# Kernel optimization log

Hardware: AMD Instinct MI355X
Metric: run time of the kernel (lower is better)

## Reference

```python
import jax, jax.numpy as jnp
import numpy as np

STAGE = 100  # number of weight bins


def _bin_reconstruct(w, affine):
    # Faithful vectorization of the 100-iter binning loop: element in bin i
    # (half-open interval) gets scaled by affine[i]; the max element falls
    # outside every bin (w < wmin + stage*range/stage fails) and is zeroed.
    flat = w.reshape(-1)
    wmin, wmax = flat.min(), flat.max()
    idx = jnp.floor((flat - wmin) / (wmax - wmin) * STAGE).astype(jnp.int32)
    mask = (idx < STAGE).astype(flat.dtype)  # mask is detached in torch (non-diff anyway)
    scale = affine[jnp.clip(idx, 0, STAGE - 1)]
    return flat * scale * mask


def _kl_vs_laplace(new_flat, lap):
    # F.kl_div(log_softmax(w), softmax(lap), reduction='none').mean()
    logq = jax.nn.log_softmax(new_flat)
    p = jax.nn.softmax(lap)
    return (p * (jnp.log(p) - logq)).mean()


def _adder2d(x, w, stride, padding, groups=1):
    # AdderNet conv: out = -sum_k |patch_k - w_k| (no bias)
    O, Cg, kh, kw = w.shape
    patches = jax.lax.conv_general_dilated_patches(
        x, (kh, kw), (stride, stride), [(padding, padding), (padding, padding)])
    B, _, Hp, Wp = patches.shape  # channel dim ordered (C, kh, kw), C-major
    if groups == 1:
        p = patches.reshape(B, 1, Cg * kh * kw, Hp, Wp)
        wf = w.reshape(1, O, Cg * kh * kw, 1, 1)
    else:  # depthwise: groups == C_in, Cg == 1, O == C_in
        p = patches.reshape(B, O, kh * kw, Hp, Wp)
        wf = w.reshape(1, O, kh * kw, 1, 1)
    return -jnp.abs(p - wf).sum(axis=2)  # [B, O, Hp, Wp]


def _bn_train(x, g, b, eps=1e-5):
    # BatchNorm2d in training mode (batch statistics, biased variance)
    m = x.mean(axis=(0, 2, 3), keepdims=True)
    v = ((x - m) ** 2).mean(axis=(0, 2, 3), keepdims=True)
    return (x - m) * jax.lax.rsqrt(v + eps) * g.reshape(1, -1, 1, 1) + b.reshape(1, -1, 1, 1)


def _forward(x, sw_ds, sw_c1, sw_c2, sw_c3, a_ds, a_c1, a_c2, a_c3, peg_w,
             g1, b1, g2, b2, g3, b3, gds, bds, lap_ds, lap_c1, lap_c2, lap_c3):
    kl = jnp.float32(0.0)
    f_ds = _bin_reconstruct(sw_ds, a_ds)
    kl = kl + _kl_vs_laplace(f_ds, lap_ds)
    f_c1 = _bin_reconstruct(sw_c1, a_c1)
    kl = kl + _kl_vs_laplace(f_c1, lap_c1)
    residual = jax.nn.relu(_bn_train(_adder2d(x, f_ds.reshape(sw_ds.shape), 1, 0), gds, bds))
    h = _adder2d(x, f_c1.reshape(sw_c1.shape), 1, 0)
    h = _adder2d(h, peg_w, 1, 1, groups=peg_w.shape[0])  # PEG depthwise 3x3
    h = jax.nn.relu(_bn_train(h, g1, b1))
    f_c2 = _bin_reconstruct(sw_c2, a_c2)
    kl = kl + _kl_vs_laplace(f_c2, lap_c2)
    h = _adder2d(h, f_c2.reshape(sw_c2.shape), 1, 1)
    h = jax.nn.relu(_bn_train(h, g2, b2))
    f_c3 = _bin_reconstruct(sw_c3, a_c3)
    kl = kl + _kl_vs_laplace(f_c3, lap_c3)
    h = _adder2d(h, f_c3.reshape(sw_c3.shape), 1, 0)
    h = _bn_train(h, g3, b3)  # bn3 gamma zero-initialized
    return jax.nn.relu(h + residual), kl


def setup_inputs() -> dict:
    key = jax.random.key(0)
    ks = jax.random.split(key, 16)
    inp = {
        'x': jax.random.normal(ks[0], (4, 128, 28, 28), jnp.float32),
        'sw_downsample': jax.random.normal(ks[1], (256, 128, 1, 1), jnp.float32) * 0.05,
        'sw_conv1': jax.random.normal(ks[2], (64, 128, 1, 1), jnp.float32) * 0.05,
        'sw_conv2': jax.random.normal(ks[3], (64, 64, 3, 3), jnp.float32) * 0.05,
        'sw_conv3': jax.random.normal(ks[4], (256, 64, 1, 1), jnp.float32) * 0.05,
        'downsample_affine': jax.random.normal(ks[5], (100,), jnp.float32),
        'conv1_affine': jax.random.normal(ks[6], (100,), jnp.float32),
        'conv2_affine': jax.random.normal(ks[7], (100,), jnp.float32),
        'conv3_affine': jax.random.normal(ks[8], (100,), jnp.float32),
        'peg_w': jax.random.normal(ks[9], (64, 1, 3, 3), jnp.float32) * 0.05,
        'bn1_g': jnp.ones((64,), jnp.float32), 'bn1_b': jnp.zeros((64,), jnp.float32),
        'bn2_g': jnp.ones((64,), jnp.float32), 'bn2_b': jnp.zeros((64,), jnp.float32),
        'bn3_g': jnp.zeros((256,), jnp.float32), 'bn3_b': jnp.zeros((256,), jnp.float32),
        'bnds_g': jnp.ones((256,), jnp.float32), 'bnds_b': jnp.zeros((256,), jnp.float32),
        # Laplace(0, 2) samples, drawn once in setup so the reference is deterministic
        'lap_ds': jax.random.laplace(ks[10], (32768,), jnp.float32) * 2.0,
        'lap_c1': jax.random.laplace(ks[11], (8192,), jnp.float32) * 2.0,
        'lap_c2': jax.random.laplace(ks[12], (36864,), jnp.float32) * 2.0,
        'lap_c3': jax.random.laplace(ks[13], (16384,), jnp.float32) * 2.0,
    }
    return inp


def reference(x, sw_downsample, sw_conv1, sw_conv2, sw_conv3,
              downsample_affine, conv1_affine, conv2_affine, conv3_affine, peg_w,
              bn1_g, bn1_b, bn2_g, bn2_b, bn3_g, bn3_b, bnds_g, bnds_b,
              lap_ds, lap_c1, lap_c2, lap_c3):
    return _forward(x, sw_downsample, sw_conv1, sw_conv2, sw_conv3,
                    downsample_affine, conv1_affine, conv2_affine, conv3_affine, peg_w,
                    bn1_g, bn1_b, bn2_g, bn2_b, bn3_g, bn3_b, bnds_g, bnds_b,
                    lap_ds, lap_c1, lap_c2, lap_c3)
```

## Files before the change

kernel.cpp:

```cpp
#include <hip/hip_runtime.h>
#include <math.h>


#define HW 784
#define NB 4
#define STAGE 100

__device__ __forceinline__ float wredSum(float v){
  for (int o = 32; o > 0; o >>= 1) v += __shfl_down(v, o, 64);
  return v;
}
__device__ __forceinline__ float wredMax(float v){
  for (int o = 32; o > 0; o >>= 1) v = fmaxf(v, __shfl_down(v, o, 64));
  return v;
}
__device__ __forceinline__ float wredMin(float v){
  for (int o = 32; o > 0; o >>= 1) v = fminf(v, __shfl_down(v, o, 64));
  return v;
}
__device__ __forceinline__ double wredSumD(double v){
  for (int o = 32; o > 0; o >>= 1) v += __shfl_down(v, o, 64);
  return v;
}

__device__ float blockMin4(float v){
  __shared__ float shn[4];
  __syncthreads();
  v = wredMin(v);
  if ((threadIdx.x & 63) == 0) shn[threadIdx.x >> 6] = v;
  __syncthreads();
  return fminf(fminf(shn[0], shn[1]), fminf(shn[2], shn[3]));
}
__device__ float blockMax4(float v){
  __shared__ float shx[4];
  __syncthreads();
  v = wredMax(v);
  if ((threadIdx.x & 63) == 0) shx[threadIdx.x >> 6] = v;
  __syncthreads();
  return fmaxf(fmaxf(shx[0], shx[1]), fmaxf(shx[2], shx[3]));
}

__device__ void stats4(float v0, float v1, float v2, float v3,
                       double* sumP, double* sqP, int oc0){
  __shared__ double sred[4][8];
  __syncthreads();
  const int w = threadIdx.x >> 6;
  float vv[4] = {v0, v1, v2, v3};
  #pragma unroll
  for (int i = 0; i < 4; i++){
    double d = (double)vv[i];
    double s = wredSumD(d);
    double q = wredSumD(d * d);
    if ((threadIdx.x & 63) == 0){ sred[w][i] = s; sred[w][4 + i] = q; }
  }
  __syncthreads();
  if (threadIdx.x < 8){
    double tot = sred[0][threadIdx.x] + sred[1][threadIdx.x]
               + sred[2][threadIdx.x] + sred[3][threadIdx.x];
    int i = threadIdx.x & 3;
    if (threadIdx.x < 4) atomicAdd(&sumP[oc0 + i], tot);
    else                 atomicAdd(&sqP[oc0 + i],  tot);
  }
}
__device__ void stats2(float v0, float v1, double* sumP, double* sqP, int oc0){
  __shared__ double sred2[4][4];
  __syncthreads();
  const int w = threadIdx.x >> 6;
  float vv[2] = {v0, v1};
  #pragma unroll
  for (int i = 0; i < 2; i++){
    double d = (double)vv[i];
    double s = wredSumD(d);
    double q = wredSumD(d * d);
    if ((threadIdx.x & 63) == 0){ sred2[w][i] = s; sred2[w][2 + i] = q; }
  }
  __syncthreads();
  if (threadIdx.x < 4){
    double tot = sred2[0][threadIdx.x] + sred2[1][threadIdx.x]
               + sred2[2][threadIdx.x] + sred2[3][threadIdx.x];
    int i = threadIdx.x & 1;
    if (threadIdx.x < 2) atomicAdd(&sumP[oc0 + i], tot);
    else                 atomicAdd(&sqP[oc0 + i],  tot);
  }
}

__device__ void klAccum(float se, float sel, float sef, float sq, double* dst){
  __shared__ double kls[4][4];
  __syncthreads();
  const int w = threadIdx.x >> 6;
  double a0 = wredSumD((double)se);
  double a1 = wredSumD((double)sel);
  double a2 = wredSumD((double)sef);
  double a3 = wredSumD((double)sq);
  if ((threadIdx.x & 63) == 0){
    kls[w][0] = a0; kls[w][1] = a1; kls[w][2] = a2; kls[w][3] = a3;
  }
  __syncthreads();
  if (threadIdx.x < 4){
    double tot = kls[0][threadIdx.x] + kls[1][threadIdx.x]
               + kls[2][threadIdx.x] + kls[3][threadIdx.x];
    atomicAdd(&dst[threadIdx.x], tot);
  }
}

__device__ __forceinline__ float reconv(float vv, float mn, float rng,
                                        const float* saff){
  float q = (vv - mn) / rng * 100.0f;
  int idx = (int)floorf(q);
  float nv = 0.0f;
  if (idx < STAGE){
    int ci = idx < 0 ? 0 : (idx > STAGE - 1 ? STAGE - 1 : idx);
    nv = vv * saff[ci];
  }
  return nv;
}

__device__ __forceinline__ void mmReduce(const float* mmbuf, int tens,
                                         float& mn, float& mx){
  mn = 3.402823466e38f; mx = -3.402823466e38f;
  #pragma unroll
  for (int k = 0; k < 16; k++){
    mn = fminf(mn, mmbuf[tens * 32 + k]);
    mx = fmaxf(mx, mmbuf[tens * 32 + 16 + k]);
  }
}

__global__ __launch_bounds__(256) void minmax_kernel(
    const float* w0, int n0, const float* w1, int n1,
    const float* w2, int n2, const float* w3, int n3,
    float* mmbuf, double* dstat)
{
  if (threadIdx.x < 21) dstat[blockIdx.x * 21 + threadIdx.x] = 0.0;
  const int tens = blockIdx.x >> 4, slot = blockIdx.x & 15;
  const float* w; int n;
  if      (tens == 0){ w = w0; n = n0; }
  else if (tens == 1){ w = w1; n = n1; }
  else if (tens == 2){ w = w2; n = n2; }
  else               { w = w3; n = n3; }
  float mn = 3.402823466e38f, mx = -3.402823466e38f;
  for (int i = slot * 256 + threadIdx.x; i < n; i += 4096){
    float v = w[i];
    mn = fminf(mn, v); mx = fmaxf(mx, v);
  }
  mn = blockMin4(mn); mx = blockMax4(mx);
  if (threadIdx.x == 0){
    mmbuf[tens * 32 + slot]      = mn;
    mmbuf[tens * 32 + 16 + slot] = mx;
  }
}

__global__ __launch_bounds__(256) void front_kernel(
    const float* __restrict__ x,
    const float* __restrict__ w_ds, const float* __restrict__ aff_ds,
    const float* __restrict__ lap_ds,
    const float* __restrict__ w_c1, const float* __restrict__ aff_c1,
    const float* __restrict__ lap_c1,
    const float* __restrict__ w_c2, const float* __restrict__ aff_c2,
    const float* __restrict__ lap_c2, float* __restrict__ f_c2,
    const float* __restrict__ w_c3, const float* __restrict__ aff_c3,
    const float* __restrict__ lap_c3,
    const float* __restrict__ peg_w, const float* __restrict__ mmbuf,
    float* __restrict__ A, float* __restrict__ T2, double* __restrict__ dS)
{
  const int t = threadIdx.x;
  if (blockIdx.x < 512){
    const int a = blockIdx.x;
    const int chunk = a & 3, og = (a >> 2) & 31, b = a >> 7;
    const int oc0 = og * 8;
    __shared__ float saff[STAGE];
    __shared__ float sw[1024];
    if (t < STAGE) saff[t] = aff_ds[t];
    float mn, mx; mmReduce(mmbuf, 0, mn, mx);
    const float rng = mx - mn;
    __syncthreads();
    for (int k = t; k < 1024; k += 256)
      sw[k] = reconv(w_ds[oc0 * 128 + k], mn, rng, saff);
    __syncthreads();

    const int px = chunk * 196 + t;
    float v0=0,v1=0,v2=0,v3=0,v4=0,v5=0,v6=0,v7=0;
    if (t < 196){
      const float* xp = x + (size_t)b * 128 * HW + px;
      float c0=0,c1=0,c2=0,c3=0,c4=0,c5=0,c6=0,c7=0;
      #pragma unroll 4
      for (int c = 0; c < 128; c++){
        float xv = xp[(size_t)c * HW];
        c0 += fabsf(xv - sw[c]);
        c1 += fabsf(xv - sw[128 + c]);
        c2 += fabsf(xv - sw[256 + c]);
        c3 += fabsf(xv - sw[384 + c]);
        c4 += fabsf(xv - sw[512 + c]);
        c5 += fabsf(xv - sw[640 + c]);
        c6 += fabsf(xv - sw[768 + c]);
        c7 += fabsf(xv - sw[896 + c]);
      }
      v0=-c0; v1=-c1; v2=-c2; v3=-c3; v4=-c4; v5=-c5; v6=-c6; v7=-c7;
      float* op = A + ((size_t)(b * 256 + oc0)) * HW + px;
      op[0]=v0; op[HW]=v1; op[2*HW]=v2; op[3*HW]=v3;
      op[4*HW]=v4; op[5*HW]=v5; op[6*HW]=v6; op[7*HW]=v7;
    }
    stats4(v0, v1, v2, v3, dS + 0, dS + 256, oc0);
    stats4(v4, v5, v6, v7, dS + 0, dS + 256, oc0 + 4);

    if (b == 0 && chunk == 0){
      float se = 0, sel = 0, sef = 0, sq = 0;
      for (int k = t; k < 1024; k += 256){
        float l = lap_ds[oc0 * 128 + k];
        float e = expf(l);
        se += e; sel += e * l; sef += e * sw[k];
        sq += expf(sw[k]);
      }
      klAccum(se, sel, sef, sq, dS + 1280 + 0);
    }
  } else if (blockIdx.x < 768){
    const int a = blockIdx.x - 512;
    const int rc = a & 3, og = (a >> 2) & 15, b = a >> 6;
    const int oc0 = og * 4;
    __shared__ float saffc[STAGE];
    __shared__ float swc[512];
    __shared__ float swp[36];
    __shared__ float sT1[4][256];
    if (t < STAGE) saffc[t] = aff_c1[t];
    if (t >= 128 && t < 164) swp[t - 128] = peg_w[oc0 * 9 + (t - 128)];
    float mn, mx; mmReduce(mmbuf, 1, mn, mx);
    const float rng = mx - mn;
    __syncthreads();
    for (int k = t; k < 512; k += 256)
      swc[k] = reconv(w_c1[oc0 * 128 + k], mn, rng, saffc);
    __syncthreads();

    if (t < 252){
      const int rr = t / 28;
      const int col = t - rr * 28;
      const int wr = rc * 7 - 1 + rr;
      float tv0 = 0, tv1 = 0, tv2 = 0, tv3 = 0;
      if (wr >= 0 && wr < 28){
        const float* xp = x + (size_t)b * 128 * HW + wr * 28 + col;
        float c0 = 0, c1 = 0, c2 = 0, c3 = 0;
        #pragma unroll 4
        for (int c = 0; c < 128; c++){
          float xv = xp[(size_t)c * HW];
          c0 += fabsf(xv - swc[c]);
          c1 += fabsf(xv - swc[128 + c]);
          c2 += fabsf(xv - swc[256 + c]);
          c3 += fabsf(xv - swc[384 + c]);
        }
        tv0 = -c0; tv1 = -c1; tv2 = -c2; tv3 = -c3;
      }
      sT1[0][t] = tv0; sT1[1][t] = tv1; sT1[2][t] = tv2; sT1[3][t] = tv3;
    }
    __syncthreads();
    float v0 = 0, v1 = 0, v2 = 0, v3 = 0;
    if (t < 196){
      const int r = t / 28, col = t - r * 28;
      float c0 = 0, c1 = 0, c2 = 0, c3 = 0;
      #pragma unroll
      for (int ky = 0; ky < 3; ky++){
        #pragma unroll
        for (int kx = 0; kx < 3; kx++){
          int cc = col + kx - 1;
          bool ok = (cc >= 0) && (cc < 28);
          int idx = ok ? ((r + ky) * 28 + cc) : 0;
          float p0 = ok ? sT1[0][idx] : 0.0f;
          float p1 = ok ? sT1[1][idx] : 0.0f;
          float p2 = ok ? sT1[2][idx] : 0.0f;
          float p3 = ok ? sT1[3][idx] : 0.0f;
          int wk = ky * 3 + kx;
          c0 += fabsf(p0 - swp[wk]);
          c1 += fabsf(p1 - swp[9 + wk]);
          c2 += fabsf(p2 - swp[18 + wk]);
          c3 += fabsf(p3 - swp[27 + wk]);
        }
      }
      v0 = -c0; v1 = -c1; v2 = -c2; v3 = -c3;
      const int opx = (rc * 7 + r) * 28 + col;
      float* op = T2 + ((size_t)(b * 64 + oc0)) * HW + opx;
      op[0] = v0; op[HW] = v1; op[2 * HW] = v2; op[3 * HW] = v3;
    }
    stats4(v0, v1, v2, v3, dS + 512, dS + 576, oc0);

    if (b == 0 && rc == 0){
      float se = 0, sel = 0, sef = 0, sq = 0;
      for (int k = t; k < 512; k += 256){
        float l = lap_c1[oc0 * 128 + k];
        float e = expf(l);
        se += e; sel += e * l; sef += e * swc[k];
        sq += expf(swc[k]);
      }
      klAccum(se, sel, sef, sq, dS + 1280 + 4);
    }
  } else if (blockIdx.x < 832){
    const int j = blockIdx.x - 768;
    __shared__ float saff2[STAGE];
    if (t < STAGE) saff2[t] = aff_c2[t];
    float mn, mx; mmReduce(mmbuf, 2, mn, mx);
    const float rng = mx - mn;
    __syncthreads();
    float se = 0, sel = 0, sef = 0, sq = 0;
    for (int k = t; k < 576; k += 256){
      float nv = reconv(w_c2[j * 576 + k], mn, rng, saff2);
      f_c2[j * 576 + k] = nv;
      float l = lap_c2[j * 576 + k];
      float e = expf(l);
      se += e; sel += e * l; sef += e * nv; sq += expf(nv);
    }
    klAccum(se, sel, sef, sq, dS + 1280 + 8);
  } else {
    const int j = blockIdx.x - 832;
    __shared__ float saff3[STAGE];
    if (t < STAGE) saff3[t] = aff_c3[t];
    float mn, mx; mmReduce(mmbuf, 3, mn, mx);
    const float rng = mx - mn;
    __syncthreads();
    float se = 0, sel = 0, sef = 0, sq = 0;
    for (int k = t; k < 1024; k += 256){
      float nv = reconv(w_c3[j * 1024 + k], mn, rng, saff3);
      float l = lap_c3[j * 1024 + k];
      float e = expf(l);
      se += e; sel += e * l; sef += e * nv; sq += expf(nv);
    }
    klAccum(se, sel, sef, sq, dS + 1280 + 12);
  }
}

__global__ __launch_bounds__(256) void bnapply_pad_kernel(
    const float* __restrict__ T2, float* __restrict__ T2b,
    const float* __restrict__ g1, const float* __restrict__ b1,
    const double* __restrict__ dS)
{
  const int a = blockIdx.x;
  const int c = a & 63, b = a >> 6;
  __shared__ float ssc, ssb;
  if (threadIdx.x == 0){
    double s  = dS[512 + c] * (1.0 / 3136.0);
    double vr = dS[576 + c] * (1.0 / 3136.0) - s * s;
    float scale = g1[c] * rsqrtf((float)vr + 1e-5f);
    ssc = scale; ssb = b1[c] - (float)s * scale;
  }
  __syncthreads();
  const float sc_ = ssc, bi_ = ssb;
  const float* src = T2 + (size_t)a * HW;
  float* dst = T2b + (size_t)a * 960;
  for (int i = threadIdx.x; i < 960; i += 256){
    int row = i >> 5, col = i & 31;
    float v = 0.0f;
    if (row >= 1 && row <= 28 && col >= 1 && col <= 28)
      v = fmaxf(src[(row - 1) * 28 + (col - 1)] * sc_ + bi_, 0.0f);
    dst[i] = v;
  }
}

__global__ __launch_bounds__(256) void mid3x3_kernel(
    const float* __restrict__ T2b, const float* __restrict__ f_c2,
    float* __restrict__ T3, double* __restrict__ dS)
{
  const int t = threadIdx.x;
  const int a = blockIdx.x;
  const int chunk = a & 3, og = (a >> 2) & 31, b = a >> 7;
  const int oc0 = og * 2;
  const float* __restrict__ wA = f_c2 + oc0 * 576;
  const float* __restrict__ wB = wA + 576;

  float v0 = 0, v1 = 0;
  const int px = chunk * 196 + t;
  if (t < 196){
    const int y = px / 28, xc = px - y * 28;
    const float* base = T2b + (size_t)b * 64 * 960 + y * 32 + xc;
    float c0 = 0, c1 = 0;
    #pragma unroll 2
    for (int c = 0; c < 64; c++){
      const float* p = base + c * 960;
      float t0 = p[0],  t1 = p[1],  t2 = p[2];
      float t3 = p[32], t4 = p[33], t5 = p[34];
      float t6 = p[64], t7 = p[65], t8 = p[66];
      const float* wa = wA + c * 9;
      const float* wb = wB + c * 9;
      c0 += fabsf(t0 - wa[0]) + fabsf(t1 - wa[1]) + fabsf(t2 - wa[2])
          + fabsf(t3 - wa[3]) + fabsf(t4 - wa[4]) + fabsf(t5 - wa[5])
          + fabsf(t6 - wa[6]) + fabsf(t7 - wa[7]) + fabsf(t8 - wa[8]);
      c1 += fabsf(t0 - wb[0]) + fabsf(t1 - wb[1]) + fabsf(t2 - wb[2])
          + fabsf(t3 - wb[3]) + fabsf(t4 - wb[4]) + fabsf(t5 - wb[5])
          + fabsf(t6 - wb[6]) + fabsf(t7 - wb[7]) + fabsf(t8 - wb[8]);
    }
    v0 = -c0; v1 = -c1;
    T3[((size_t)(b * 64 + oc0)) * HW + px]     = v0;
    T3[((size_t)(b * 64 + oc0 + 1)) * HW + px] = v1;
  }
  stats2(v0, v1, dS + 640, dS + 704, oc0);
}

__global__ __launch_bounds__(256) void back_kernel(
    const float* __restrict__ T3, const float* __restrict__ w_c3,
    const float* __restrict__ aff_c3, const float* __restrict__ mmbuf,
    const float* __restrict__ g2, const float* __restrict__ b2,
    float* __restrict__ out, double* __restrict__ dS)
{
  const int t = threadIdx.x;
  const int a = blockIdx.x;
  const int chunk = a & 3, og = (a >> 2) & 63, b = a >> 8;
  const int oc0 = og * 4;
  __shared__ float ssc[64], ssb[64], sw[256], saff[STAGE];
  if (t < 64){
    double s  = dS[640 + t] * (1.0 / 3136.0);
    double vr = dS[704 + t] * (1.0 / 3136.0) - s * s;
    float scale = g2[t] * rsqrtf((float)vr + 1e-5f);
    ssc[t] = scale; ssb[t] = b2[t] - (float)s * scale;
  }
  if (t >= 128 && t < 128 + STAGE) saff[t - 128] = aff_c3[t - 128];
  float mn, mx; mmReduce(mmbuf, 3, mn, mx);
  const float rng = mx - mn;
  __syncthreads();
  sw[t] = reconv(w_c3[oc0 * 64 + t], mn, rng, saff);
  __syncthreads();

  const int px = chunk * 196 + t;
  float v0 = 0, v1 = 0, v2 = 0, v3 = 0;
  if (t < 196){
    const float* bp = T3 + (size_t)b * 64 * HW + px;
    float c0 = 0, c1 = 0, c2 = 0, c3 = 0;
    #pragma unroll 4
    for (int c = 0; c < 64; c++){
      float raw = bp[(size_t)c * HW];
      float vv = fmaxf(raw * ssc[c] + ssb[c], 0.0f);
      c0 += fabsf(vv - sw[c]);
      c1 += fabsf(vv - sw[64 + c]);
      c2 += fabsf(vv - sw[128 + c]);
      c3 += fabsf(vv - sw[192 + c]);
    }
    v0 = -c0; v1 = -c1; v2 = -c2; v3 = -c3;
    float* op = out + ((size_t)(b * 256 + oc0)) * HW + px;
    op[0] = v0; op[HW] = v1; op[2 * HW] = v2; op[3 * HW] = v3;
  }
  stats4(v0, v1, v2, v3, dS + 768, dS + 1024, oc0);
}

__global__ __launch_bounds__(256) void final_kernel(
    float* __restrict__ out, const float* __restrict__ A,
    const float* __restrict__ g3, const float* __restrict__ b3,
    const float* __restrict__ gds, const float* __restrict__ bds,
    const double* __restrict__ dS)
{
  __shared__ float s3c[256], s3b[256], sdc[256], sdb[256];
  const int t = threadIdx.x;
  {
    double s  = dS[768 + t] * (1.0 / 3136.0);
    double vr = dS[1024 + t] * (1.0 / 3136.0) - s * s;
    float scale = g3[t] * rsqrtf((float)vr + 1e-5f);
    s3c[t] = scale; s3b[t] = b3[t] - (float)s * scale;
    s  = dS[t] * (1.0 / 3136.0);
    vr = dS[256 + t] * (1.0 / 3136.0) - s * s;
    scale = gds[t] * rsqrtf((float)vr + 1e-5f);
    sdc[t] = scale; sdb[t] = bds[t] - (float)s * scale;
  }
  __syncthreads();
  #pragma unroll
  for (int k = 0; k < 4; k++){
    int n = blockIdx.x * 1024 + k * 256 + t;
    int c = (n / HW) & 255;
    float h = out[n], aa = A[n];
    float r = fmaxf(aa * sdc[c] + sdb[c], 0.0f);
    out[n] = fmaxf(h * s3c[c] + s3b[c] + r, 0.0f);
  }
  if (blockIdx.x == 0 && t == 0){
    const int ns[4] = {32768, 8192, 36864, 16384};
    float kl = 0.0f;
    #pragma unroll
    for (int q = 0; q < 4; q++){
      double se  = dS[1280 + q * 4];
      double sel = dS[1280 + q * 4 + 1];
      double sef = dS[1280 + q * 4 + 2];
      double sq  = dS[1280 + q * 4 + 3];
      kl += (float)((((sel - sef) / se) - log(se) + log(sq)) / (double)ns[q]);
    }
    out[802816] = kl;
  }
}

extern "C" void kernel_launch(void* const* d_in, const int* in_sizes, int n_in,
                              void* d_out, int out_size, void* d_ws, size_t ws_size,
                              hipStream_t stream)
{
  const float* x      = (const float*)d_in[0];
  const float* sw_ds  = (const float*)d_in[1];
  const float* sw_c1  = (const float*)d_in[2];
  const float* sw_c2  = (const float*)d_in[3];
  const float* sw_c3  = (const float*)d_in[4];
  const float* a_ds   = (const float*)d_in[5];
  const float* a_c1   = (const float*)d_in[6];
  const float* a_c2   = (const float*)d_in[7];
  const float* a_c3   = (const float*)d_in[8];
  const float* peg_w  = (const float*)d_in[9];
  const float* bn1_g  = (const float*)d_in[10];
  const float* bn1_b  = (const float*)d_in[11];
  const float* bn2_g  = (const float*)d_in[12];
  const float* bn2_b  = (const float*)d_in[13];
  const float* bn3_g  = (const float*)d_in[14];
  const float* bn3_b  = (const float*)d_in[15];
  const float* bnds_g = (const float*)d_in[16];
  const float* bnds_b = (const float*)d_in[17];
  const float* lap_ds = (const float*)d_in[18];
  const float* lap_c1 = (const float*)d_in[19];
  const float* lap_c2 = (const float*)d_in[20];
  const float* lap_c3 = (const float*)d_in[21];

  float* ws    = (float*)d_ws;
  float* f_c2  = ws;
  float* mmbuf = ws + 36864;
  double* dstat= (double*)(ws + 37120);
  float* A     = ws + 39808;
  float* T2    = ws + 842624;
  float* T3    = ws + 1043328;
  float* T2b   = ws + 1244032;

  float* out = (float*)d_out;

  minmax_kernel<<<64, 256, 0, stream>>>(
      sw_ds, 32768, sw_c1, 8192, sw_c2, 36864, sw_c3, 16384, mmbuf, dstat);

  front_kernel<<<848, 256, 0, stream>>>(
      x, sw_ds, a_ds, lap_ds, sw_c1, a_c1, lap_c1,
      sw_c2, a_c2, lap_c2, f_c2, sw_c3, a_c3, lap_c3,
      peg_w, mmbuf, A, T2, dstat);

  bnapply_pad_kernel<<<256, 256, 0, stream>>>(T2, T2b, bn1_g, bn1_b, dstat);

  mid3x3_kernel<<<512, 256, 0, stream>>>(T2b, f_c2, T3, dstat);

  back_kernel<<<1024, 256, 0, stream>>>(T3, sw_c3, a_c3, mmbuf,
                                        bn2_g, bn2_b, out, dstat);

  final_kernel<<<784, 256, 0, stream>>>(out, A, bn3_g, bn3_b, bnds_g, bnds_b,
                                        dstat);
}
```

Measured before the change: 171.8 us.

## Precompute reconstructed weights once in transposed layout and drop per-block requantization

Replaces the min/max kernel with one kernel that computes each weight tensor's full min/max per block, reconstructs the binned weights once, stores them transposed (input-channel-major) in workspace, and writes per-block KL partial sums without atomics. The conv kernels now read the transposed weights straight from global memory instead of rebuilding them in shared memory in every block. This removes redundant reconstruction work and several barriers per block. In exchange, every block of the reconstruction kernel rescans its whole tensor for min/max, and the inner loops take uniform global loads in place of LDS reads, which relies on caching.

```diff
diff --git a/kernel.cpp b/kernel.cpp
--- a/kernel.cpp
+++ b/kernel.cpp
@@ -6,10 +6,6 @@
 #define NB 4
 #define STAGE 100
 
-__device__ __forceinline__ float wredSum(float v){
-  for (int o = 32; o > 0; o >>= 1) v += __shfl_down(v, o, 64);
-  return v;
-}
 __device__ __forceinline__ float wredMax(float v){
   for (int o = 32; o > 0; o >>= 1) v = fmaxf(v, __shfl_down(v, o, 64));
   return v;
@@ -84,25 +80,6 @@
   }
 }
 
-__device__ void klAccum(float se, float sel, float sef, float sq, double* dst){
-  __shared__ double kls[4][4];
-  __syncthreads();
-  const int w = threadIdx.x >> 6;
-  double a0 = wredSumD((double)se);
-  double a1 = wredSumD((double)sel);
-  double a2 = wredSumD((double)sef);
-  double a3 = wredSumD((double)sq);
-  if ((threadIdx.x & 63) == 0){
-    kls[w][0] = a0; kls[w][1] = a1; kls[w][2] = a2; kls[w][3] = a3;
-  }
-  __syncthreads();
-  if (threadIdx.x < 4){
-    double tot = kls[0][threadIdx.x] + kls[1][threadIdx.x]
-               + kls[2][threadIdx.x] + kls[3][threadIdx.x];
-    atomicAdd(&dst[threadIdx.x], tot);
-  }
-}
-
 __device__ __forceinline__ float reconv(float vv, float mn, float rng,
                                         const float* saff){
   float q = (vv - mn) / rng * 100.0f;
@@ -115,51 +92,75 @@
   return nv;
 }
 
-__device__ __forceinline__ void mmReduce(const float* mmbuf, int tens,
-                                         float& mn, float& mx){
-  mn = 3.402823466e38f; mx = -3.402823466e38f;
-  #pragma unroll
-  for (int k = 0; k < 16; k++){
-    mn = fminf(mn, mmbuf[tens * 32 + k]);
-    mx = fmaxf(mx, mmbuf[tens * 32 + 16 + k]);
-  }
-}
-
-__global__ __launch_bounds__(256) void minmax_kernel(
-    const float* w0, int n0, const float* w1, int n1,
-    const float* w2, int n2, const float* w3, int n3,
-    float* mmbuf, double* dstat)
-{
-  if (threadIdx.x < 21) dstat[blockIdx.x * 21 + threadIdx.x] = 0.0;
-  const int tens = blockIdx.x >> 4, slot = blockIdx.x & 15;
-  const float* w; int n;
-  if      (tens == 0){ w = w0; n = n0; }
-  else if (tens == 1){ w = w1; n = n1; }
-  else if (tens == 2){ w = w2; n = n2; }
-  else               { w = w3; n = n3; }
+__global__ __launch_bounds__(256) void reconkl_kernel(
+    const float* __restrict__ w_ds, const float* __restrict__ a_ds,
+    const float* __restrict__ lap_ds, float* __restrict__ f_dsT,
+    const float* __restrict__ w_c1, const float* __restrict__ a_c1,
+    const float* __restrict__ lap_c1, float* __restrict__ f_c1T,
+    const float* __restrict__ w_c2, const float* __restrict__ a_c2,
+    const float* __restrict__ lap_c2, float* __restrict__ f_c2,
+    const float* __restrict__ w_c3, const float* __restrict__ a_c3,
+    const float* __restrict__ lap_c3, float* __restrict__ f_c3T,
+    double* __restrict__ dstat)
+{
+  const int blk = blockIdx.x, t = threadIdx.x;
+  if (t < 14 && blk * 14 + t < 1280) dstat[blk * 14 + t] = 0.0;
+
+  int tens, slice;
+  if      (blk < 32){ tens = 0; slice = blk; }
+  else if (blk < 40){ tens = 1; slice = blk - 32; }
+  else if (blk < 76){ tens = 2; slice = blk - 40; }
+  else              { tens = 3; slice = blk - 76; }
+  const float *w, *aff, *lap; int n;
+  if      (tens == 0){ w = w_ds; aff = a_ds; lap = lap_ds; n = 32768; }
+  else if (tens == 1){ w = w_c1; aff = a_c1; lap = lap_c1; n = 8192; }
+  else if (tens == 2){ w = w_c2; aff = a_c2; lap = lap_c2; n = 36864; }
+  else               { w = w_c3; aff = a_c3; lap = lap_c3; n = 16384; }
+
+  __shared__ float saff[STAGE];
+  if (t < STAGE) saff[t] = aff[t];
+
+  const float4* w4 = (const float4*)w;
   float mn = 3.402823466e38f, mx = -3.402823466e38f;
-  for (int i = slot * 256 + threadIdx.x; i < n; i += 4096){
-    float v = w[i];
-    mn = fminf(mn, v); mx = fmaxf(mx, v);
+  for (int i = t; i < (n >> 2); i += 256){
+    float4 v = w4[i];
+    mn = fminf(mn, fminf(fminf(v.x, v.y), fminf(v.z, v.w)));
+    mx = fmaxf(mx, fmaxf(fmaxf(v.x, v.y), fmaxf(v.z, v.w)));
   }
   mn = blockMin4(mn); mx = blockMax4(mx);
-  if (threadIdx.x == 0){
-    mmbuf[tens * 32 + slot]      = mn;
-    mmbuf[tens * 32 + 16 + slot] = mx;
+  const float rng = mx - mn;
+
+  float se = 0, sel = 0, sef = 0, sq = 0;
+  const int k0 = slice * 1024;
+  for (int j = t; j < 1024; j += 256){
+    int k = k0 + j;
+    float nv = reconv(w[k], mn, rng, saff);
+    if      (tens == 0){ int oc = k >> 7, c = k & 127; f_dsT[c * 256 + oc] = nv; }
+    else if (tens == 1){ int oc = k >> 7, c = k & 127; f_c1T[c * 64 + oc] = nv; }
+    else if (tens == 2){ f_c2[k] = nv; }
+    else               { int oc = k >> 6, c = k & 63;  f_c3T[c * 256 + oc] = nv; }
+    float l = lap[k];
+    float e = expf(l);
+    se += e; sel += e * l; sef += e * nv; sq += expf(nv);
+  }
+  __shared__ double kls[4][4];
+  __syncthreads();
+  const int wv = t >> 6;
+  double a0 = wredSumD((double)se);
+  double a1 = wredSumD((double)sel);
+  double a2 = wredSumD((double)sef);
+  double a3 = wredSumD((double)sq);
+  if ((t & 63) == 0){ kls[wv][0]=a0; kls[wv][1]=a1; kls[wv][2]=a2; kls[wv][3]=a3; }
+  __syncthreads();
+  if (t < 4){
+    double tot = kls[0][t] + kls[1][t] + kls[2][t] + kls[3][t];
+    dstat[1280 + blk * 4 + t] = tot;
   }
 }
 
 __global__ __launch_bounds__(256) void front_kernel(
-    const float* __restrict__ x,
-    const float* __restrict__ w_ds, const float* __restrict__ aff_ds,
-    const float* __restrict__ lap_ds,
-    const float* __restrict__ w_c1, const float* __restrict__ aff_c1,
-    const float* __restrict__ lap_c1,
-    const float* __restrict__ w_c2, const float* __restrict__ aff_c2,
-    const float* __restrict__ lap_c2, float* __restrict__ f_c2,
-    const float* __restrict__ w_c3, const float* __restrict__ aff_c3,
-    const float* __restrict__ lap_c3,
-    const float* __restrict__ peg_w, const float* __restrict__ mmbuf,
+    const float* __restrict__ x, const float* __restrict__ f_dsT,
+    const float* __restrict__ f_c1T, const float* __restrict__ peg_w,
     float* __restrict__ A, float* __restrict__ T2, double* __restrict__ dS)
 {
   const int t = threadIdx.x;
@@ -167,32 +168,24 @@
     const int a = blockIdx.x;
     const int chunk = a & 3, og = (a >> 2) & 31, b = a >> 7;
     const int oc0 = og * 8;
-    __shared__ float saff[STAGE];
-    __shared__ float sw[1024];
-    if (t < STAGE) saff[t] = aff_ds[t];
-    float mn, mx; mmReduce(mmbuf, 0, mn, mx);
-    const float rng = mx - mn;
-    __syncthreads();
-    for (int k = t; k < 1024; k += 256)
-      sw[k] = reconv(w_ds[oc0 * 128 + k], mn, rng, saff);
-    __syncthreads();
-
     const int px = chunk * 196 + t;
     float v0=0,v1=0,v2=0,v3=0,v4=0,v5=0,v6=0,v7=0;
     if (t < 196){
       const float* xp = x + (size_t)b * 128 * HW + px;
+      const float* wp = f_dsT + oc0;
       float c0=0,c1=0,c2=0,c3=0,c4=0,c5=0,c6=0,c7=0;
       #pragma unroll 4
       for (int c = 0; c < 128; c++){
         float xv = xp[(size_t)c * HW];
-        c0 += fabsf(xv - sw[c]);
-        c1 += fabsf(xv - sw[128 + c]);
-        c2 += fabsf(xv - sw[256 + c]);
-        c3 += fabsf(xv - sw[384 + c]);
-        c4 += fabsf(xv - sw[512 + c]);
-        c5 += fabsf(xv - sw[640 + c]);
-        c6 += fabsf(xv - sw[768 + c]);
-        c7 += fabsf(xv - sw[896 + c]);
+        const float* wr = wp + c * 256;
+        c0 += fabsf(xv - wr[0]);
+        c1 += fabsf(xv - wr[1]);
+        c2 += fabsf(xv - wr[2]);
+        c3 += fabsf(xv - wr[3]);
+        c4 += fabsf(xv - wr[4]);
+        c5 += fabsf(xv - wr[5]);
+        c6 += fabsf(xv - wr[6]);
+        c7 += fabsf(xv - wr[7]);
       }
       v0=-c0; v1=-c1; v2=-c2; v3=-c3; v4=-c4; v5=-c5; v6=-c6; v7=-c7;
       float* op = A + ((size_t)(b * 256 + oc0)) * HW + px;
@@ -201,34 +194,11 @@
     }
     stats4(v0, v1, v2, v3, dS + 0, dS + 256, oc0);
     stats4(v4, v5, v6, v7, dS + 0, dS + 256, oc0 + 4);
-
-    if (b == 0 && chunk == 0){
-      float se = 0, sel = 0, sef = 0, sq = 0;
-      for (int k = t; k < 1024; k += 256){
-        float l = lap_ds[oc0 * 128 + k];
-        float e = expf(l);
-        se += e; sel += e * l; sef += e * sw[k];
-        sq += expf(sw[k]);
-      }
-      klAccum(se, sel, sef, sq, dS + 1280 + 0);
-    }
-  } else if (blockIdx.x < 768){
+  } else {
     const int a = blockIdx.x - 512;
     const int rc = a & 3, og = (a >> 2) & 15, b = a >> 6;
     const int oc0 = og * 4;
-    __shared__ float saffc[STAGE];
-    __shared__ float swc[512];
-    __shared__ float swp[36];
     __shared__ float sT1[4][256];
-    if (t < STAGE) saffc[t] = aff_c1[t];
-    if (t >= 128 && t < 164) swp[t - 128] = peg_w[oc0 * 9 + (t - 128)];
-    float mn, mx; mmReduce(mmbuf, 1, mn, mx);
-    const float rng = mx - mn;
-    __syncthreads();
-    for (int k = t; k < 512; k += 256)
-      swc[k] = reconv(w_c1[oc0 * 128 + k], mn, rng, saffc);
-    __syncthreads();
-
     if (t < 252){
       const int rr = t / 28;
       const int col = t - rr * 28;
@@ -236,14 +206,16 @@
       float tv0 = 0, tv1 = 0, tv2 = 0, tv3 = 0;
       if (wr >= 0 && wr < 28){
         const float* xp = x + (size_t)b * 128 * HW + wr * 28 + col;
+        const float* wp = f_c1T + oc0;
         float c0 = 0, c1 = 0, c2 = 0, c3 = 0;
         #pragma unroll 4
         for (int c = 0; c < 128; c++){
           float xv = xp[(size_t)c * HW];
-          c0 += fabsf(xv - swc[c]);
-          c1 += fabsf(xv - swc[128 + c]);
-          c2 += fabsf(xv - swc[256 + c]);
-          c3 += fabsf(xv - swc[384 + c]);
+          const float* wrp = wp + c * 64;
+          c0 += fabsf(xv - wrp[0]);
+          c1 += fabsf(xv - wrp[1]);
+          c2 += fabsf(xv - wrp[2]);
+          c3 += fabsf(xv - wrp[3]);
         }
         tv0 = -c0; tv1 = -c1; tv2 = -c2; tv3 = -c3;
       }
@@ -253,6 +225,10 @@
     float v0 = 0, v1 = 0, v2 = 0, v3 = 0;
     if (t < 196){
       const int r = t / 28, col = t - r * 28;
+      const float* wp0 = peg_w + oc0 * 9;
+      const float* wp1 = wp0 + 9;
+      const float* wp2 = wp0 + 18;
+      const float* wp3 = wp0 + 27;
       float c0 = 0, c1 = 0, c2 = 0, c3 = 0;
       #pragma unroll
       for (int ky = 0; ky < 3; ky++){
@@ -266,10 +242,10 @@
           float p2 = ok ? sT1[2][idx] : 0.0f;
           float p3 = ok ? sT1[3][idx] : 0.0f;
           int wk = ky * 3 + kx;
-          c0 += fabsf(p0 - swp[wk]);
-          c1 += fabsf(p1 - swp[9 + wk]);
-          c2 += fabsf(p2 - swp[18 + wk]);
-          c3 += fabsf(p3 - swp[27 + wk]);
+          c0 += fabsf(p0 - wp0[wk]);
+          c1 += fabsf(p1 - wp1[wk]);
+          c2 += fabsf(p2 - wp2[wk]);
+          c3 += fabsf(p3 - wp3[wk]);
         }
       }
       v0 = -c0; v1 = -c1; v2 = -c2; v3 = -c3;
@@ -278,48 +254,6 @@
       op[0] = v0; op[HW] = v1; op[2 * HW] = v2; op[3 * HW] = v3;
     }
     stats4(v0, v1, v2, v3, dS + 512, dS + 576, oc0);
-
-    if (b == 0 && rc == 0){
-      float se = 0, sel = 0, sef = 0, sq = 0;
-      for (int k = t; k < 512; k += 256){
-        float l = lap_c1[oc0 * 128 + k];
-        float e = expf(l);
-        se += e; sel += e * l; sef += e * swc[k];
-        sq += expf(swc[k]);
-      }
-      klAccum(se, sel, sef, sq, dS + 1280 + 4);
-    }
-  } else if (blockIdx.x < 832){
-    const int j = blockIdx.x - 768;
-    __shared__ float saff2[STAGE];
-    if (t < STAGE) saff2[t] = aff_c2[t];
-    float mn, mx; mmReduce(mmbuf, 2, mn, mx);
-    const float rng = mx - mn;
-    __syncthreads();
-    float se = 0, sel = 0, sef = 0, sq = 0;
-    for (int k = t; k < 576; k += 256){
-      float nv = reconv(w_c2[j * 576 + k], mn, rng, saff2);
-      f_c2[j * 576 + k] = nv;
-      float l = lap_c2[j * 576 + k];
-      float e = expf(l);
-      se += e; sel += e * l; sef += e * nv; sq += expf(nv);
-    }
-    klAccum(se, sel, sef, sq, dS + 1280 + 8);
-  } else {
-    const int j = blockIdx.x - 832;
-    __shared__ float saff3[STAGE];
-    if (t < STAGE) saff3[t] = aff_c3[t];
-    float mn, mx; mmReduce(mmbuf, 3, mn, mx);
-    const float rng = mx - mn;
-    __syncthreads();
-    float se = 0, sel = 0, sef = 0, sq = 0;
-    for (int k = t; k < 1024; k += 256){
-      float nv = reconv(w_c3[j * 1024 + k], mn, rng, saff3);
-      float l = lap_c3[j * 1024 + k];
-      float e = expf(l);
-      se += e; sel += e * l; sef += e * nv; sq += expf(nv);
-    }
-    klAccum(se, sel, sef, sq, dS + 1280 + 12);
   }
 }
 
@@ -329,7 +263,7 @@
     const double* __restrict__ dS)
 {
   const int a = blockIdx.x;
-  const int c = a & 63, b = a >> 6;
+  const int c = a & 63;
   __shared__ float ssc, ssb;
   if (threadIdx.x == 0){
     double s  = dS[512 + c] * (1.0 / 3136.0);
@@ -390,8 +324,7 @@
 }
 
 __global__ __launch_bounds__(256) void back_kernel(
-    const float* __restrict__ T3, const float* __restrict__ w_c3,
-    const float* __restrict__ aff_c3, const float* __restrict__ mmbuf,
+    const float* __restrict__ T3, const float* __restrict__ f_c3T,
     const float* __restrict__ g2, const float* __restrict__ b2,
     float* __restrict__ out, double* __restrict__ dS)
 {
@@ -399,33 +332,30 @@
   const int a = blockIdx.x;
   const int chunk = a & 3, og = (a >> 2) & 63, b = a >> 8;
   const int oc0 = og * 4;
-  __shared__ float ssc[64], ssb[64], sw[256], saff[STAGE];
+  __shared__ float ssc[64], ssb[64];
   if (t < 64){
     double s  = dS[640 + t] * (1.0 / 3136.0);
     double vr = dS[704 + t] * (1.0 / 3136.0) - s * s;
     float scale = g2[t] * rsqrtf((float)vr + 1e-5f);
     ssc[t] = scale; ssb[t] = b2[t] - (float)s * scale;
   }
-  if (t >= 128 && t < 128 + STAGE) saff[t - 128] = aff_c3[t - 128];
-  float mn, mx; mmReduce(mmbuf, 3, mn, mx);
-  const float rng = mx - mn;
-  __syncthreads();
-  sw[t] = reconv(w_c3[oc0 * 64 + t], mn, rng, saff);
   __syncthreads();
 
   const int px = chunk * 196 + t;
   float v0 = 0, v1 = 0, v2 = 0, v3 = 0;
   if (t < 196){
     const float* bp = T3 + (size_t)b * 64 * HW + px;
+    const float* wp = f_c3T + oc0;
     float c0 = 0, c1 = 0, c2 = 0, c3 = 0;
     #pragma unroll 4
     for (int c = 0; c < 64; c++){
       float raw = bp[(size_t)c * HW];
       float vv = fmaxf(raw * ssc[c] + ssb[c], 0.0f);
-      c0 += fabsf(vv - sw[c]);
-      c1 += fabsf(vv - sw[64 + c]);
-      c2 += fabsf(vv - sw[128 + c]);
-      c3 += fabsf(vv - sw[192 + c]);
+      const float* wr = wp + c * 256;
+      c0 += fabsf(vv - wr[0]);
+      c1 += fabsf(vv - wr[1]);
+      c2 += fabsf(vv - wr[2]);
+      c3 += fabsf(vv - wr[3]);
     }
     v0 = -c0; v1 = -c1; v2 = -c2; v3 = -c3;
     float* op = out + ((size_t)(b * 256 + oc0)) * HW + px;
@@ -461,18 +391,30 @@
     float r = fmaxf(aa * sdc[c] + sdb[c], 0.0f);
     out[n] = fmaxf(h * s3c[c] + s3b[c] + r, 0.0f);
   }
-  if (blockIdx.x == 0 && t == 0){
-    const int ns[4] = {32768, 8192, 36864, 16384};
-    float kl = 0.0f;
-    #pragma unroll
-    for (int q = 0; q < 4; q++){
-      double se  = dS[1280 + q * 4];
-      double sel = dS[1280 + q * 4 + 1];
-      double sef = dS[1280 + q * 4 + 2];
-      double sq  = dS[1280 + q * 4 + 3];
-      kl += (float)((((sel - sef) / se) - log(se) + log(sq)) / (double)ns[q]);
-    }
-    out[802816] = kl;
+  if (blockIdx.x == 0){
+    __shared__ double klsh[92][4];
+    if (t < 92){
+      klsh[t][0] = dS[1280 + t * 4];
+      klsh[t][1] = dS[1280 + t * 4 + 1];
+      klsh[t][2] = dS[1280 + t * 4 + 2];
+      klsh[t][3] = dS[1280 + t * 4 + 3];
+    }
+    __syncthreads();
+    if (t == 0){
+      const int lo[4] = {0, 32, 40, 76};
+      const int hi[4] = {32, 40, 76, 92};
+      const int ns[4] = {32768, 8192, 36864, 16384};
+      float kl = 0.0f;
+      for (int q = 0; q < 4; q++){
+        double se = 0, sel = 0, sef = 0, sq = 0;
+        for (int j = lo[q]; j < hi[q]; j++){
+          se += klsh[j][0]; sel += klsh[j][1];
+          sef += klsh[j][2]; sq += klsh[j][3];
+        }
+        kl += (float)((((sel - sef) / se) - log(se) + log(sq)) / (double)ns[q]);
+      }
+      out[802816] = kl;
+    }
   }
 }
 
@@ -504,30 +446,31 @@
   const float* lap_c3 = (const float*)d_in[21];
 
   float* ws    = (float*)d_ws;
-  float* f_c2  = ws;
-  float* mmbuf = ws + 36864;
-  double* dstat= (double*)(ws + 37120);
-  float* A     = ws + 39808;
-  float* T2    = ws + 842624;
-  float* T3    = ws + 1043328;
-  float* T2b   = ws + 1244032;
+  float* f_dsT = ws;
+  float* f_c1T = ws + 32768;
+  float* f_c2  = ws + 40960;
+  float* f_c3T = ws + 77824;
+  double* dstat= (double*)(ws + 94208);
+  float* A     = ws + 98304;
+  float* T2    = ws + 901120;
+  float* T3    = ws + 1101824;
+  float* T2b   = ws + 1302528;
 
   float* out = (float*)d_out;
 
-  minmax_kernel<<<64, 256, 0, stream>>>(
-      sw_ds, 32768, sw_c1, 8192, sw_c2, 36864, sw_c3, 16384, mmbuf, dstat);
-
-  front_kernel<<<848, 256, 0, stream>>>(
-      x, sw_ds, a_ds, lap_ds, sw_c1, a_c1, lap_c1,
-      sw_c2, a_c2, lap_c2, f_c2, sw_c3, a_c3, lap_c3,
-      peg_w, mmbuf, A, T2, dstat);
+  reconkl_kernel<<<92, 256, 0, stream>>>(
+      sw_ds, a_ds, lap_ds, f_dsT,
+      sw_c1, a_c1, lap_c1, f_c1T,
+      sw_c2, a_c2, lap_c2, f_c2,
+      sw_c3, a_c3, lap_c3, f_c3T, dstat);
+
+  front_kernel<<<768, 256, 0, stream>>>(x, f_dsT, f_c1T, peg_w, A, T2, dstat);
 
   bnapply_pad_kernel<<<256, 256, 0, stream>>>(T2, T2b, bn1_g, bn1_b, dstat);
 
   mid3x3_kernel<<<512, 256, 0, stream>>>(T2b, f_c2, T3, dstat);
 
-  back_kernel<<<1024, 256, 0, stream>>>(T3, sw_c3, a_c3, mmbuf,
-                                        bn2_g, bn2_b, out, dstat);
+  back_kernel<<<1024, 256, 0, stream>>>(T3, f_c3T, bn2_g, bn2_b, out, dstat);
 
   final_kernel<<<784, 256, 0, stream>>>(out, A, bn3_g, bn3_b, bnds_g, bnds_b,
                                         dstat);
```

Result: slower. 181.0 us (+5.3%).
